# Kernel optimization log

Hardware: AMD Instinct MI355X
Metric: run time of the kernel (lower is better)

Reference implementation:

```python
import jax, jax.numpy as jnp
import numpy as np

DIM = 3            # point feature dim (xyz)
POS_HID = 64       # pos_mlp hidden
ATTN_HID = DIM * 4 # attn_mlp hidden (mult=4)
N_NBR = 16         # points per group
GROUPS = 512       # groups per batch element
MLP_D = N_NBR * DIM  # 48


def setup_inputs() -> dict:
    key = jax.random.key(0)
    ks = jax.random.split(key, 20)
    B = 32
    s = lambda *sh: 1.0 / np.sqrt(sh[0])
    inp = {
        "original_points": jax.random.normal(ks[0], (B, GROUPS, DIM), jnp.float32),
        "data": jax.random.normal(ks[1], (B, GROUPS, N_NBR, DIM), jnp.float32),
        # PointTransformerLayer params
        "w_qkv": jax.random.normal(ks[2], (DIM, DIM * 3), jnp.float32) * s(DIM),
        "pos_w1": jax.random.normal(ks[3], (3, POS_HID), jnp.float32) * s(3),
        "pos_b1": jnp.zeros((POS_HID,), jnp.float32),
        "pos_w2": jax.random.normal(ks[4], (POS_HID, DIM), jnp.float32) * s(POS_HID),
        "pos_b2": jnp.zeros((DIM,), jnp.float32),
        "attn_w1": jax.random.normal(ks[5], (DIM, ATTN_HID), jnp.float32) * s(DIM),
        "attn_b1": jnp.zeros((ATTN_HID,), jnp.float32),
        "attn_w2": jax.random.normal(ks[6], (ATTN_HID, DIM), jnp.float32) * s(ATTN_HID),
        "attn_b2": jnp.zeros((DIM,), jnp.float32),
        # downstream MLP params
        "mlp_w1": jax.random.normal(ks[7], (MLP_D, MLP_D), jnp.float32) * s(MLP_D),
        "mlp_b1": jnp.zeros((MLP_D,), jnp.float32),
        "mlp_w2": jax.random.normal(ks[8], (MLP_D, MLP_D), jnp.float32) * s(MLP_D),
        "mlp_b2": jnp.zeros((MLP_D,), jnp.float32),
        "mlp_w3": jax.random.normal(ks[9], (MLP_D, 1), jnp.float32) * s(MLP_D),
        "mlp_b3": jnp.zeros((1,), jnp.float32),
    }
    return inp


def reference(original_points, data, w_qkv, pos_w1, pos_b1, pos_w2, pos_b2,
              attn_w1, attn_b1, attn_w2, attn_b2,
              mlp_w1, mlp_b1, mlp_w2, mlp_b2, mlp_w3, mlp_b3):
    B, G, n, d = data.shape
    x = data.reshape(B * G, n, d)          # (BG, n, 3)
    pos = x[:, :, :3]                       # pos == features here (f=3)

    # Point-transformer vector attention
    qkv = x @ w_qkv                          # (BG, n, 9)
    q, k, v = jnp.split(qkv, 3, axis=-1)
    rel_pos = pos[:, :, None, :] - pos[:, None, :, :]              # (BG, n, n, 3)
    rel_emb = jax.nn.relu(rel_pos @ pos_w1 + pos_b1) @ pos_w2 + pos_b2  # (BG, n, n, 3)
    qk_rel = q[:, :, None, :] - k[:, None, :, :]                   # (BG, n, n, 3)
    v_ij = v[:, None, :, :] + rel_emb                              # (BG, n, n, 3)
    sim = jax.nn.relu((qk_rel + rel_emb) @ attn_w1 + attn_b1) @ attn_w2 + attn_b2
    attn = jax.nn.softmax(sim, axis=-2)                            # softmax over j
    agg = jnp.einsum('bijd,bijd->bid', attn, v_ij)                 # (BG, n, 3)

    # regroup into (B, 512, 48) exactly as stack(split(512, dim=0))
    sa = agg.reshape(B, G, n * d)
    h = jax.nn.relu(sa @ mlp_w1 + mlp_b1)
    h = jax.nn.relu(h @ mlp_w2 + mlp_b2)
    return h @ mlp_w3 + mlp_b3              # (B, 512, 1)
```

## Files before the change

### kernel.cpp

```cpp
#include <hip/hip_runtime.h>


typedef _Float16 h2 __attribute__((ext_vector_type(2)));
typedef _Float16 h8 __attribute__((ext_vector_type(8)));

#define AH_STRIDE 36

union H8U { h8 v; h2 p[4]; unsigned u[4]; };

__device__ __forceinline__ h2 pkrtz(float a, float b) {
    return __builtin_bit_cast(h2, __builtin_amdgcn_cvt_pkrtz(a, b));
}
__device__ __forceinline__ h2 uash2(unsigned u) {
    return __builtin_bit_cast(h2, u);
}
__device__ __forceinline__ h2 hmax2(h2 a, h2 b) {
    return __builtin_elementwise_max(a, b);
}

#if __has_builtin(__builtin_amdgcn_fdot2)
__device__ __forceinline__ float dot2acc(h2 a, h2 b, float c) {
    return __builtin_amdgcn_fdot2(a, b, c, false);
}
#else
__device__ __forceinline__ float dot2acc(h2 a, h2 b, float c) {
    float d;
    asm("v_dot2_f32_f16 %0, %1, %2, %3"
        : "=v"(d)
        : "v"(__builtin_bit_cast(int, a)), "v"(__builtin_bit_cast(int, b)), "v"(c));
    return d;
}
#endif

__device__ __forceinline__ float dpp_add16(float x) {
    float s = x;
    int t;
    t = __builtin_amdgcn_update_dpp(0, __builtin_bit_cast(int, s), 0x121, 0xf, 0xf, false);
    s += __builtin_bit_cast(float, t);
    t = __builtin_amdgcn_update_dpp(0, __builtin_bit_cast(int, s), 0x122, 0xf, 0xf, false);
    s += __builtin_bit_cast(float, t);
    t = __builtin_amdgcn_update_dpp(0, __builtin_bit_cast(int, s), 0x124, 0xf, 0xf, false);
    s += __builtin_bit_cast(float, t);
    t = __builtin_amdgcn_update_dpp(0, __builtin_bit_cast(int, s), 0x128, 0xf, 0xf, false);
    s += __builtin_bit_cast(float, t);
    return s;
}

__global__ void wpack(const float* __restrict__ pw2, const float* __restrict__ aw1,
                      const float* __restrict__ ab1, const float* __restrict__ aw2,
                      unsigned* __restrict__ ws) {
    const int t = threadIdx.x;
    const float L2E = 1.44269504f;
    if (t < 96) {
        const int hp = t & 31, c = t >> 5;
        ws[c*32+hp] = __builtin_bit_cast(unsigned, pkrtz(pw2[(2*hp)*3+c], pw2[(2*hp+1)*3+c]));
    } else if (t < 114) {
        const int idx = t - 96, r = idx / 6, gp = idx % 6;
        ws[96+r*6+gp] = __builtin_bit_cast(unsigned, pkrtz(aw1[r*12+2*gp], aw1[r*12+2*gp+1]));
    } else if (t < 120) {
        const int gp = t - 114;
        ws[114+gp] = __builtin_bit_cast(unsigned, pkrtz(ab1[2*gp], ab1[2*gp+1]));
    } else if (t < 138) {
        const int idx = t - 120, gp = idx / 3, c = idx % 3;
        ws[120+gp*3+c] = __builtin_bit_cast(unsigned,
            pkrtz(aw2[(2*gp)*3+c] * L2E, aw2[(2*gp+1)*3+c] * L2E));
    }
}

__global__ __launch_bounds__(64, 8) void pt_main(
    const float* __restrict__ data,
    const float* __restrict__ wqkv,
    const float* __restrict__ pw1,
    const float* __restrict__ pb1,
    const float* __restrict__ pb2,
    const float* __restrict__ ab2,
    const float* __restrict__ mw1,
    const float* __restrict__ mb1,
    const float* __restrict__ mw2,
    const float* __restrict__ mb2,
    const float* __restrict__ mw3,
    const float* __restrict__ mb3,
    const unsigned* __restrict__ wsp,
    float* __restrict__ out)
{
    __shared__ __attribute__((aligned(16))) float s_q4[64], s_k4[64], s_v4[64];
    __shared__ __attribute__((aligned(16))) float s_sa[48];
    __shared__ __attribute__((aligned(16))) float s_h1[48];
    __shared__ __attribute__((aligned(16))) unsigned s_a1h[16 * AH_STRIDE];
    __shared__ __attribute__((aligned(16))) unsigned s_a2h[16 * AH_STRIDE];

    const int ln = threadIdx.x;
    const int g  = blockIdx.x;

    if (ln < 48) {
        const int sec = ln >> 4, p = ln & 15;
        const float x0 = data[g*48 + p*3 + 0];
        const float x1 = data[g*48 + p*3 + 1];
        const float x2 = data[g*48 + p*3 + 2];
        float* dst = (sec == 0) ? s_q4 : (sec == 1) ? s_k4 : s_v4;
        #pragma unroll
        for (int c = 0; c < 3; ++c) {
            dst[p*4+c] = fmaf(x0, wqkv[0*9 + sec*3 + c],
                         fmaf(x1, wqkv[1*9 + sec*3 + c],
                         x2 * wqkv[2*9 + sec*3 + c]));
        }
        dst[p*4+3] = 0.0f;
    }

    {
        const int p  = ln & 15;
        const int qd = ln >> 4;
        const int hc = qd << 4;
        const float x0 = data[g*48 + p*3 + 0];
        const float x1 = data[g*48 + p*3 + 1];
        const float x2 = data[g*48 + p*3 + 2];
        float s[16];
        #pragma unroll
        for (int c = 0; c < 16; ++c) {
            const int h = hc + c;
            s[c] = fmaf(x0, pw1[h], fmaf(x1, pw1[64+h], x2 * pw1[128+h]));
        }
        uint4 a1u0, a1u1, a2u0, a2u1;
        #pragma unroll
        for (int d = 0; d < 4; ++d) {
            const int c = d * 2;
            (&a1u0.x)[d] = __builtin_bit_cast(unsigned, pkrtz(s[c]   + pb1[hc+c],   s[c+1] + pb1[hc+c+1]));
            (&a1u1.x)[d] = __builtin_bit_cast(unsigned, pkrtz(s[8+c] + pb1[hc+8+c], s[9+c] + pb1[hc+9+c]));
            (&a2u0.x)[d] = __builtin_bit_cast(unsigned, pkrtz(s[c],   s[c+1]));
            (&a2u1.x)[d] = __builtin_bit_cast(unsigned, pkrtz(s[8+c], s[9+c]));
        }
        const int base = p * AH_STRIDE + (qd << 3);
        *(uint4*)&s_a1h[base]     = a1u0;
        *(uint4*)&s_a1h[base + 4] = a1u1;
        *(uint4*)&s_a2h[base]     = a2u0;
        *(uint4*)&s_a2h[base + 4] = a2u1;
    }
    __builtin_amdgcn_wave_barrier();

    const int j = ln & 15, q = ln >> 4;
    const float4 kv = *(const float4*)&s_k4[j*4];
    const float4 vv = *(const float4*)&s_v4[j*4];
    const h2 z2 = {(_Float16)0, (_Float16)0};
    const float L2E = 1.44269504f;
    const float mb_0 = ab2[0] * L2E, mb_1 = ab2[1] * L2E, mb_2 = ab2[2] * L2E;

    H8U ajr[8];
    #pragma unroll
    for (int cc = 0; cc < 8; ++cc)
        ajr[cc].v = *(const h8*)&s_a2h[j * AH_STRIDE + cc*4];

    #pragma unroll
    for (int half = 0; half < 2; ++half) {
        const int iA = q + 8*half, iB = iA + 4;

        float eA0 = pb2[0], eA1 = pb2[1], eA2 = pb2[2];
        float eB0 = pb2[0], eB1 = pb2[1], eB2 = pb2[2];
        #pragma unroll
        for (int cc = 0; cc < 8; ++cc) {
            H8U aiA, aiB;
            aiA.v = *(const h8*)&s_a1h[iA * AH_STRIDE + cc*4];
            aiB.v = *(const h8*)&s_a1h[iB * AH_STRIDE + cc*4];
            #pragma unroll
            for (int m = 0; m < 4; ++m) {
                const int hp = cc*4 + m;
                const h2 w0 = uash2(wsp[0*32+hp]);
                const h2 w1 = uash2(wsp[1*32+hp]);
                const h2 w2 = uash2(wsp[2*32+hp]);
                h2 rA = hmax2(aiA.p[m] - ajr[cc].p[m], z2);
                h2 rB = hmax2(aiB.p[m] - ajr[cc].p[m], z2);
                eA0 = dot2acc(rA, w0, eA0);
                eA1 = dot2acc(rA, w1, eA1);
                eA2 = dot2acc(rA, w2, eA2);
                eB0 = dot2acc(rB, w0, eB0);
                eB1 = dot2acc(rB, w1, eB1);
                eB2 = dot2acc(rB, w2, eB2);
            }
        }

        const float4 qA = *(const float4*)&s_q4[iA*4];
        const float4 qB = *(const float4*)&s_q4[iB*4];

        const float viA0 = vv.x + eA0, viA1 = vv.y + eA1, viA2 = vv.z + eA2;
        const float viB0 = vv.x + eB0, viB1 = vv.y + eB1, viB2 = vv.z + eB2;
        const float siA0 = qA.x - kv.x + eA0, siA1 = qA.y - kv.y + eA1, siA2 = qA.z - kv.z + eA2;
        const float siB0 = qB.x - kv.x + eB0, siB1 = qB.y - kv.y + eB1, siB2 = qB.z - kv.z + eB2;

        const h2 sAx = pkrtz(siA0, siA0), sAy = pkrtz(siA1, siA1), sAz = pkrtz(siA2, siA2);
        const h2 sBx = pkrtz(siB0, siB0), sBy = pkrtz(siB1, siB1), sBz = pkrtz(siB2, siB2);
        float mA0 = mb_0, mA1 = mb_1, mA2 = mb_2;
        float mB0 = mb_0, mB1 = mb_1, mB2 = mb_2;
        #pragma unroll
        for (int gp = 0; gp < 6; ++gp) {
            const h2 b1p = uash2(wsp[114+gp]);
            const h2 u0 = uash2(wsp[96+0*6+gp]);
            const h2 u1 = uash2(wsp[96+1*6+gp]);
            const h2 u2 = uash2(wsp[96+2*6+gp]);
            const h2 v0 = uash2(wsp[120+gp*3+0]);
            const h2 v1 = uash2(wsp[120+gp*3+1]);
            const h2 v2 = uash2(wsp[120+gp*3+2]);
            h2 accA = b1p, accB = b1p;
            accA = __builtin_elementwise_fma(sAx, u0, accA);
            accA = __builtin_elementwise_fma(sAy, u1, accA);
            accA = __builtin_elementwise_fma(sAz, u2, accA);
            accB = __builtin_elementwise_fma(sBx, u0, accB);
            accB = __builtin_elementwise_fma(sBy, u1, accB);
            accB = __builtin_elementwise_fma(sBz, u2, accB);
            h2 hA = hmax2(accA, z2), hB = hmax2(accB, z2);
            mA0 = dot2acc(hA, v0, mA0);
            mA1 = dot2acc(hA, v1, mA1);
            mA2 = dot2acc(hA, v2, mA2);
            mB0 = dot2acc(hB, v0, mB0);
            mB1 = dot2acc(hB, v1, mB1);
            mB2 = dot2acc(hB, v2, mB2);
        }

        const float pA0 = __builtin_amdgcn_exp2f(mA0);
        const float pA1 = __builtin_amdgcn_exp2f(mA1);
        const float pA2 = __builtin_amdgcn_exp2f(mA2);
        const float pB0 = __builtin_amdgcn_exp2f(mB0);
        const float pB1 = __builtin_amdgcn_exp2f(mB1);
        const float pB2 = __builtin_amdgcn_exp2f(mB2);

        const float nA0 = dpp_add16(pA0 * viA0);
        const float nA1 = dpp_add16(pA1 * viA1);
        const float nA2 = dpp_add16(pA2 * viA2);
        const float dA0 = dpp_add16(pA0);
        const float dA1 = dpp_add16(pA1);
        const float dA2 = dpp_add16(pA2);
        const float nB0 = dpp_add16(pB0 * viB0);
        const float nB1 = dpp_add16(pB1 * viB1);
        const float nB2 = dpp_add16(pB2 * viB2);
        const float dB0 = dpp_add16(pB0);
        const float dB1 = dpp_add16(pB1);
        const float dB2 = dpp_add16(pB2);

        if (j == 0) {
            s_sa[iA*3+0] = nA0 * __builtin_amdgcn_rcpf(dA0);
            s_sa[iA*3+1] = nA1 * __builtin_amdgcn_rcpf(dA1);
            s_sa[iA*3+2] = nA2 * __builtin_amdgcn_rcpf(dA2);
            s_sa[iB*3+0] = nB0 * __builtin_amdgcn_rcpf(dB0);
            s_sa[iB*3+1] = nB1 * __builtin_amdgcn_rcpf(dB1);
            s_sa[iB*3+2] = nB2 * __builtin_amdgcn_rcpf(dB2);
        }
    }
    __builtin_amdgcn_wave_barrier();

    if (ln < 48) {
        const int o = ln;
        float a0 = 0.f, a1 = 0.f, a2 = 0.f, a3 = 0.f;
        #pragma unroll
        for (int c = 0; c < 48; c += 4) {
            const float4 sa = *(const float4*)&s_sa[c];
            a0 = fmaf(sa.x, mw1[(c+0)*48+o], a0);
            a1 = fmaf(sa.y, mw1[(c+1)*48+o], a1);
            a2 = fmaf(sa.z, mw1[(c+2)*48+o], a2);
            a3 = fmaf(sa.w, mw1[(c+3)*48+o], a3);
        }
        s_h1[o] = fmaxf((a0+a1) + (a2+a3) + mb1[o], 0.0f);
        __builtin_amdgcn_wave_barrier();
        float b0 = 0.f, b1 = 0.f, b2 = 0.f, b3 = 0.f;
        #pragma unroll
        for (int c = 0; c < 48; c += 4) {
            const float4 hh = *(const float4*)&s_h1[c];
            b0 = fmaf(hh.x, mw2[(c+0)*48+o], b0);
            b1 = fmaf(hh.y, mw2[(c+1)*48+o], b1);
            b2 = fmaf(hh.z, mw2[(c+2)*48+o], b2);
            b3 = fmaf(hh.w, mw2[(c+3)*48+o], b3);
        }
        const float h2v = fmaxf((b0+b1) + (b2+b3) + mb2[o], 0.0f);
        const float fv = h2v * mw3[o];
        const float r = dpp_add16(fv);
        const int ri = __builtin_bit_cast(int, r);
        const float tot =
            __builtin_bit_cast(float, __builtin_amdgcn_readlane(ri, 0)) +
            __builtin_bit_cast(float, __builtin_amdgcn_readlane(ri, 16)) +
            __builtin_bit_cast(float, __builtin_amdgcn_readlane(ri, 32));
        if (o == 0) out[g] = tot + mb3[0];
    }
}

extern "C" void kernel_launch(void* const* d_in, const int* in_sizes, int n_in,
                              void* d_out, int out_size, void* d_ws, size_t ws_size,
                              hipStream_t stream) {
    const float* data = (const float*)d_in[1];
    unsigned* ws = (unsigned*)d_ws;
    const int groups = out_size;

    wpack<<<1, 256, 0, stream>>>(
        (const float*)d_in[5],
        (const float*)d_in[7],
        (const float*)d_in[8],
        (const float*)d_in[9],
        ws);

    pt_main<<<groups, 64, 0, stream>>>(
        data,
        (const float*)d_in[2],
        (const float*)d_in[3],
        (const float*)d_in[4],
        (const float*)d_in[6],
        (const float*)d_in[10],
        (const float*)d_in[11],
        (const float*)d_in[12],
        (const float*)d_in[13],
        (const float*)d_in[14],
        (const float*)d_in[15],
        (const float*)d_in[16],
        ws,
        (float*)d_out);
}
```

Before: 137.4 us.

## Pre-transpose MLP weights in workspace and restructure pos-hidden precompute per hidden unit

The weight-pack kernel now also writes transposed copies of mlp_w1 and mlp_w2 into the workspace. This lets each output lane of the MLP read its weight row with contiguous float4 loads instead of 48 strided scalar loads. The pos_mlp first-layer precompute is remapped so each lane owns one hidden unit and loops over 16 points, writing half-precision values to shared memory. That cuts per-lane weight loads but uses 16-bit scattered LDS stores and repeated data loads. The pack kernel launches 9 blocks instead of 1, which adds a little launch work.

```diff
diff --git a/kernel.cpp b/kernel.cpp
--- a/kernel.cpp
+++ b/kernel.cpp
@@ -5,6 +5,8 @@
 typedef _Float16 h8 __attribute__((ext_vector_type(8)));
 
 #define AH_STRIDE 36
+#define MW1T_OFF  256
+#define MW2T_OFF 2560
 
 union H8U { h8 v; h2 p[4]; unsigned u[4]; };
 
@@ -48,22 +50,31 @@
 
 __global__ void wpack(const float* __restrict__ pw2, const float* __restrict__ aw1,
                       const float* __restrict__ ab1, const float* __restrict__ aw2,
+                      const float* __restrict__ mw1, const float* __restrict__ mw2,
                       unsigned* __restrict__ ws) {
     const int t = threadIdx.x;
     const float L2E = 1.44269504f;
-    if (t < 96) {
-        const int hp = t & 31, c = t >> 5;
-        ws[c*32+hp] = __builtin_bit_cast(unsigned, pkrtz(pw2[(2*hp)*3+c], pw2[(2*hp+1)*3+c]));
-    } else if (t < 114) {
-        const int idx = t - 96, r = idx / 6, gp = idx % 6;
-        ws[96+r*6+gp] = __builtin_bit_cast(unsigned, pkrtz(aw1[r*12+2*gp], aw1[r*12+2*gp+1]));
-    } else if (t < 120) {
-        const int gp = t - 114;
-        ws[114+gp] = __builtin_bit_cast(unsigned, pkrtz(ab1[2*gp], ab1[2*gp+1]));
-    } else if (t < 138) {
-        const int idx = t - 120, gp = idx / 3, c = idx % 3;
-        ws[120+gp*3+c] = __builtin_bit_cast(unsigned,
-            pkrtz(aw2[(2*gp)*3+c] * L2E, aw2[(2*gp+1)*3+c] * L2E));
+    if (blockIdx.x == 0) {
+        if (t < 96) {
+            const int hp = t & 31, c = t >> 5;
+            ws[c*32+hp] = __builtin_bit_cast(unsigned, pkrtz(pw2[(2*hp)*3+c], pw2[(2*hp+1)*3+c]));
+        } else if (t < 114) {
+            const int idx = t - 96, r = idx / 6, gp = idx % 6;
+            ws[96+r*6+gp] = __builtin_bit_cast(unsigned, pkrtz(aw1[r*12+2*gp], aw1[r*12+2*gp+1]));
+        } else if (t < 120) {
+            const int gp = t - 114;
+            ws[114+gp] = __builtin_bit_cast(unsigned, pkrtz(ab1[2*gp], ab1[2*gp+1]));
+        } else if (t < 138) {
+            const int idx = t - 120, gp = idx / 3, c = idx % 3;
+            ws[120+gp*3+c] = __builtin_bit_cast(unsigned,
+                pkrtz(aw2[(2*gp)*3+c] * L2E, aw2[(2*gp+1)*3+c] * L2E));
+        }
+    }
+    const int idx = blockIdx.x * 256 + t;
+    if (idx < 2304) {
+        const int o = idx / 48, c = idx % 48;
+        ws[MW1T_OFF + idx] = __builtin_bit_cast(unsigned, mw1[c*48+o]);
+        ws[MW2T_OFF + idx] = __builtin_bit_cast(unsigned, mw2[c*48+o]);
     }
 }
 
@@ -74,9 +85,7 @@
     const float* __restrict__ pb1,
     const float* __restrict__ pb2,
     const float* __restrict__ ab2,
-    const float* __restrict__ mw1,
     const float* __restrict__ mb1,
-    const float* __restrict__ mw2,
     const float* __restrict__ mb2,
     const float* __restrict__ mw3,
     const float* __restrict__ mb3,
@@ -108,32 +117,23 @@
     }
 
     {
-        const int p  = ln & 15;
-        const int qd = ln >> 4;
-        const int hc = qd << 4;
-        const float x0 = data[g*48 + p*3 + 0];
-        const float x1 = data[g*48 + p*3 + 1];
-        const float x2 = data[g*48 + p*3 + 2];
-        float s[16];
-        #pragma unroll
-        for (int c = 0; c < 16; ++c) {
-            const int h = hc + c;
-            s[c] = fmaf(x0, pw1[h], fmaf(x1, pw1[64+h], x2 * pw1[128+h]));
-        }
-        uint4 a1u0, a1u1, a2u0, a2u1;
-        #pragma unroll
-        for (int d = 0; d < 4; ++d) {
-            const int c = d * 2;
-            (&a1u0.x)[d] = __builtin_bit_cast(unsigned, pkrtz(s[c]   + pb1[hc+c],   s[c+1] + pb1[hc+c+1]));
-            (&a1u1.x)[d] = __builtin_bit_cast(unsigned, pkrtz(s[8+c] + pb1[hc+8+c], s[9+c] + pb1[hc+9+c]));
-            (&a2u0.x)[d] = __builtin_bit_cast(unsigned, pkrtz(s[c],   s[c+1]));
-            (&a2u1.x)[d] = __builtin_bit_cast(unsigned, pkrtz(s[8+c], s[9+c]));
-        }
-        const int base = p * AH_STRIDE + (qd << 3);
-        *(uint4*)&s_a1h[base]     = a1u0;
-        *(uint4*)&s_a1h[base + 4] = a1u1;
-        *(uint4*)&s_a2h[base]     = a2u0;
-        *(uint4*)&s_a2h[base + 4] = a2u1;
+        const int h = ln;
+        const float w0 = pw1[h];
+        const float w1 = pw1[64 + h];
+        const float w2 = pw1[128 + h];
+        const float bb = pb1[h];
+        unsigned short* a1s = (unsigned short*)s_a1h;
+        unsigned short* a2s = (unsigned short*)s_a2h;
+        #pragma unroll
+        for (int pp = 0; pp < 16; ++pp) {
+            const float x0 = data[g*48 + pp*3 + 0];
+            const float x1 = data[g*48 + pp*3 + 1];
+            const float x2 = data[g*48 + pp*3 + 2];
+            const float s = fmaf(x0, w0, fmaf(x1, w1, x2 * w2));
+            const unsigned u = __builtin_bit_cast(unsigned, pkrtz(s + bb, s));
+            a1s[pp*(AH_STRIDE*2) + h] = (unsigned short)u;
+            a2s[pp*(AH_STRIDE*2) + h] = (unsigned short)(u >> 16);
+        }
     }
     __builtin_amdgcn_wave_barrier();
 
@@ -247,14 +247,17 @@
 
     if (ln < 48) {
         const int o = ln;
+        const float* wT1 = (const float*)(wsp + MW1T_OFF) + o*48;
+        const float* wT2 = (const float*)(wsp + MW2T_OFF) + o*48;
         float a0 = 0.f, a1 = 0.f, a2 = 0.f, a3 = 0.f;
         #pragma unroll
         for (int c = 0; c < 48; c += 4) {
             const float4 sa = *(const float4*)&s_sa[c];
-            a0 = fmaf(sa.x, mw1[(c+0)*48+o], a0);
-            a1 = fmaf(sa.y, mw1[(c+1)*48+o], a1);
-            a2 = fmaf(sa.z, mw1[(c+2)*48+o], a2);
-            a3 = fmaf(sa.w, mw1[(c+3)*48+o], a3);
+            const float4 w  = *(const float4*)&wT1[c];
+            a0 = fmaf(sa.x, w.x, a0);
+            a1 = fmaf(sa.y, w.y, a1);
+            a2 = fmaf(sa.z, w.z, a2);
+            a3 = fmaf(sa.w, w.w, a3);
         }
         s_h1[o] = fmaxf((a0+a1) + (a2+a3) + mb1[o], 0.0f);
         __builtin_amdgcn_wave_barrier();
@@ -262,10 +265,11 @@
         #pragma unroll
         for (int c = 0; c < 48; c += 4) {
             const float4 hh = *(const float4*)&s_h1[c];
-            b0 = fmaf(hh.x, mw2[(c+0)*48+o], b0);
-            b1 = fmaf(hh.y, mw2[(c+1)*48+o], b1);
-            b2 = fmaf(hh.z, mw2[(c+2)*48+o], b2);
-            b3 = fmaf(hh.w, mw2[(c+3)*48+o], b3);
+            const float4 w  = *(const float4*)&wT2[c];
+            b0 = fmaf(hh.x, w.x, b0);
+            b1 = fmaf(hh.y, w.y, b1);
+            b2 = fmaf(hh.z, w.z, b2);
+            b3 = fmaf(hh.w, w.w, b3);
         }
         const float h2v = fmaxf((b0+b1) + (b2+b3) + mb2[o], 0.0f);
         const float fv = h2v * mw3[o];
@@ -286,11 +290,13 @@
     unsigned* ws = (unsigned*)d_ws;
     const int groups = out_size;
 
-    wpack<<<1, 256, 0, stream>>>(
+    wpack<<<9, 256, 0, stream>>>(
         (const float*)d_in[5],
         (const float*)d_in[7],
         (const float*)d_in[8],
         (const float*)d_in[9],
+        (const float*)d_in[11],
+        (const float*)d_in[13],
         ws);
 
     pt_main<<<groups, 64, 0, stream>>>(
@@ -300,9 +306,7 @@
         (const float*)d_in[4],
         (const float*)d_in[6],
         (const float*)d_in[10],
-        (const float*)d_in[11],
         (const float*)d_in[12],
-        (const float*)d_in[13],
         (const float*)d_in[14],
         (const float*)d_in[15],
         (const float*)d_in[16],
```

Result: no change. 138.3 us (+0.6%).
